# Kernel tuning notes

Hardware: AMD Instinct MI355X
Metric: run time of the kernel (lower is better)

## Reference

```python
import jax, jax.numpy as jnp
import numpy as np
from jax import lax

MAX_T = 1.0
MAX_Z = float(np.e)  # exp(MAX_T)
BITS = 8


def weight_quantization(w):
    # tanh -> scale by max-abs (no grad through alpha) -> clamp -> round with STE
    w = jnp.tanh(w)
    alpha = lax.stop_gradient(jnp.max(jnp.abs(w)))
    q = 2 ** (BITS - 1) - 1
    w = jnp.clip(w / alpha, -1.0, 1.0) * q
    w = w + lax.stop_gradient(jnp.round(w) - w)
    return w * alpha / q


def t_linear_c(inp, W, max_spike_time):
    # inp: [B, L, Fin], W: [Fout, Fin] -> out: [B, L, Fout]
    idx = jnp.argsort(inp, axis=-1)                              # [B,L,Fin]
    s_inp = jnp.take_along_axis(inp, idx, axis=-1)[..., None]    # [B,L,Fin,1]
    w_sorted = W.T[idx]                                          # [B,L,Fin,Fout]
    w_sorted = weight_quantization(w_sorted)
    mul = s_inp * w_sorted
    w_sum = jnp.cumsum(w_sorted, axis=-2)
    iw_sum = jnp.cumsum(mul, axis=-2)
    out_all = iw_sum / jnp.clip(w_sum - 1.0, 1e-10, 1e10)
    o = jnp.where(w_sum < 1.0, max_spike_time, out_all)
    o = jnp.where(o < s_inp, max_spike_time, o)
    nxt = jnp.concatenate([s_inp[:, :, 1:, :], jnp.ones_like(s_inp[:, :, :1, :])], axis=2)
    o = jnp.where(o > nxt, max_spike_time, o)
    return jnp.min(o, axis=-2)


def t_linear(inp, W, max_spike_time):
    # inp: [B, Fin], W: [Fout, Fin] -> out: [B, Fout]
    idx = jnp.argsort(inp, axis=-1)
    s_inp = jnp.take_along_axis(inp, idx, axis=-1)[..., None]    # [B,Fin,1]
    w_sorted = W.T[idx]                                          # [B,Fin,Fout]
    mul = s_inp * w_sorted
    w_sum = jnp.cumsum(w_sorted, axis=1)
    iw_sum = jnp.cumsum(mul, axis=1)
    out_all = iw_sum / jnp.clip(w_sum - 1.0, 1e-10, 1e10)
    o = jnp.where(w_sum < 1.0, max_spike_time, out_all)
    o = jnp.where(o < s_inp, max_spike_time, o)
    nxt = jnp.concatenate([s_inp[:, 1:, :], jnp.ones_like(s_inp[:, :1, :])], axis=1)
    o = jnp.where(o >= nxt, max_spike_time, o)  # note: >= in t_Linear (vs > in t_Linear_c)
    return jnp.min(o, axis=1)


def unfold(x, k, p, s):
    # torch F.unfold: zero-pad, extract kxk patches; feature order (C, kh, kw)
    B, C, H, W = x.shape
    xp = jnp.pad(x, ((0, 0), (0, 0), (p, p), (p, p)))
    oh = (H + 2 * p - k) // s + 1
    ow = (W + 2 * p - k) // s + 1
    ri = (jnp.arange(oh) * s)[:, None] + jnp.arange(k)           # [oh,k]
    ci = (jnp.arange(ow) * s)[:, None] + jnp.arange(k)           # [ow,k]
    pt = xp[:, :, ri[:, None, :, None], ci[None, :, None, :]]    # [B,C,oh,ow,k,k]
    pt = pt.transpose(0, 2, 3, 1, 4, 5).reshape(B, oh * ow, C * k * k)
    return pt, oh, ow


def t_conv(x, W, k, pad, stride, max_spike_time):
    B = x.shape[0]
    patches, oh, ow = unfold(x, k, pad, stride)                  # [B,L,C*k*k]
    patches = jnp.where(patches < 0.1, max_spike_time, patches)
    out = t_linear_c(patches, W, max_spike_time)                 # [B,L,Cout]
    return out.transpose(0, 2, 1).reshape(B, W.shape[0], oh, ow)


def max_pool2(x):
    return lax.reduce_window(x, -jnp.inf, lax.max, (1, 1, 2, 2), (1, 1, 2, 2), 'VALID')


def min_pool3(x):
    # -MaxPool3x3(stride 2)(-ConstantPad2d(1, 1e5)(x))
    xp = jnp.pad(x, ((0, 0), (0, 0), (1, 1), (1, 1)), constant_values=1e5)
    return -lax.reduce_window(-xp, -jnp.inf, lax.max, (1, 1, 3, 3), (1, 1, 2, 2), 'VALID')


def setup_inputs() -> dict:
    key = jax.random.key(0)
    ks = jax.random.split(key, 8)
    B = 8
    inp = jax.random.normal(ks[0], (B, 1, 64, 64), dtype=jnp.float32)
    conv1_w = jax.random.normal(ks[1], (32, 1, 5, 5), dtype=jnp.float32) * (1.0 / 5.0)
    bn_g = jnp.ones((32,), jnp.float32)
    bn_b = jnp.zeros((32,), jnp.float32)
    bn_m = jnp.zeros((32,), jnp.float32)
    bn_v = jnp.ones((32,), jnp.float32)
    def uw(k, fout, fin):
        return jax.random.uniform(k, (fout, fin), jnp.float32, 0.0, 10.0 / fin)
    w2 = uw(ks[2], 32, 3 * 3 * 32)
    w3 = uw(ks[3], 32, 3 * 3 * 32)
    w4 = uw(ks[4], 64, 3 * 3 * 32)
    w5 = uw(ks[5], 64, 3 * 3 * 64)
    w_fc = uw(ks[6], 10, 8 * 8 * 64)
    return {"inp": inp, "conv1_w": conv1_w, "bn_g": bn_g, "bn_b": bn_b,
            "bn_m": bn_m, "bn_v": bn_v, "w2": w2, "w3": w3, "w4": w4,
            "w5": w5, "w_fc": w_fc}


def reference(inp, conv1_w, bn_g, bn_b, bn_m, bn_v, w2, w3, w4, w5, w_fc):
    x = lax.conv_general_dilated(inp, conv1_w, (1, 1), ((2, 2), (2, 2)),
                                 dimension_numbers=('NCHW', 'OIHW', 'NCHW'))
    x = (x - bn_m[None, :, None, None]) * (bn_g / jnp.sqrt(bn_v + 1e-5))[None, :, None, None] \
        + bn_b[None, :, None, None]
    x = jax.nn.relu(x)
    x = max_pool2(x)                       # [B,32,32,32]
    x = jnp.minimum(x, MAX_T)
    z1 = jnp.exp(x)
    z2 = t_conv(z1, w2, 3, 1, 2, MAX_Z)    # [B,32,16,16]
    z3 = t_conv(z2, w3, 3, 1, 1, MAX_Z)    # [B,32,16,16]
    z3c = z3 * min_pool3(z1)
    z4 = t_conv(z3c, w4, 3, 1, 2, MAX_Z * 2)  # [B,64,8,8]
    z5 = t_conv(z4, w5, 3, 1, 1, MAX_Z * 2)   # [B,64,8,8]
    pm = min_pool3(z3c)                       # [B,32,8,8]
    pm = jnp.concatenate([pm, pm], axis=1)    # [B,64,8,8]
    z5c = (z5 * pm).reshape(z5.shape[0], -1)  # [B,4096]
    return t_linear(z5c, w_fc, MAX_Z * 4)     # [B,10]
```

## Files before the change

kernel.cpp:

```cpp
#include <hip/hip_runtime.h>
#include <hip/hip_bf16.h>
#include <math.h>

#define E32 2.7182817459106445f

__device__ __forceinline__ unsigned long long packkey(float vf, int idx) {
  unsigned u = __float_as_uint(vf);
  u = (u & 0x80000000u) ? ~u : (u | 0x80000000u);
  return (((unsigned long long)u) << 32) | (unsigned)idx;
}
__device__ __forceinline__ float unpackval(unsigned long long k) {
  unsigned m = (unsigned)(k >> 32);
  m = (m & 0x80000000u) ? (m ^ 0x80000000u) : ~m;
  return __uint_as_float(m);
}

__global__ __launch_bounds__(256) void tanh_max_kernel(
    const float* __restrict__ w2, const float* __restrict__ w3,
    const float* __restrict__ w4, const float* __restrict__ w5,
    float* __restrict__ tanhbuf, float* __restrict__ partials) {
  int blk = blockIdx.x;
  const float* w; int base_blk, tbase;
  if (blk < 36)       { w = w2; base_blk = 0;   tbase = 0; }
  else if (blk < 72)  { w = w3; base_blk = 36;  tbase = 9216; }
  else if (blk < 144) { w = w4; base_blk = 72;  tbase = 18432; }
  else                { w = w5; base_blk = 144; tbase = 36864; }
  int i = (blk - base_blk) * 256 + threadIdx.x;
  float t = tanhf(w[i]);
  tanhbuf[tbase + i] = t;
  __shared__ float red[256];
  red[threadIdx.x] = fabsf(t);
  __syncthreads();
  for (int s = 128; s > 0; s >>= 1) {
    if (threadIdx.x < s) red[threadIdx.x] = fmaxf(red[threadIdx.x], red[threadIdx.x + s]);
    __syncthreads();
  }
  if (threadIdx.x == 0) partials[blk] = red[0];
}

__global__ __launch_bounds__(256) void quant2_kernel(
    const float* __restrict__ tanhbuf, const float* __restrict__ partials,
    float* __restrict__ q2, float* __restrict__ q3,
    float* __restrict__ q4, float* __restrict__ q5) {
  int blk = blockIdx.x;
  float* dst; int base_blk, tbase, pb0, pb1, F, N;
  if (blk < 36)       { dst = q2; base_blk = 0;   tbase = 0;     pb0 = 0;   pb1 = 36;  F = 32; N = 288; }
  else if (blk < 72)  { dst = q3; base_blk = 36;  tbase = 9216;  pb0 = 36;  pb1 = 72;  F = 32; N = 288; }
  else if (blk < 144) { dst = q4; base_blk = 72;  tbase = 18432; pb0 = 72;  pb1 = 144; F = 64; N = 288; }
  else                { dst = q5; base_blk = 144; tbase = 36864; pb0 = 144; pb1 = 288; F = 64; N = 576; }
  __shared__ float red[256];
  float mx = 0.0f;
  for (int j = pb0 + threadIdx.x; j < pb1; j += 256) mx = fmaxf(mx, partials[j]);
  red[threadIdx.x] = mx;
  __syncthreads();
  for (int s = 128; s > 0; s >>= 1) {
    if (threadIdx.x < s) red[threadIdx.x] = fmaxf(red[threadIdx.x], red[threadIdx.x + s]);
    __syncthreads();
  }
  float a = red[0];
  int i = (blk - base_blk) * 256 + threadIdx.x;
  float t = tanhbuf[tbase + i];
  int f = i / N, n = i % N;
  float r = fminf(fmaxf(t / a, -1.0f), 1.0f) * 127.0f;
  dst[n * F + f] = rintf(r) * a / 127.0f;
}

__global__ __launch_bounds__(256) void transpose_wfc_kernel(
    const float* __restrict__ wfc, float* __restrict__ wfcT) {
  int o = blockIdx.x * 256 + threadIdx.x;
  if (o >= 40960) return;
  int n = o / 10, f = o % 10;
  wfcT[o] = wfc[f * 4096 + n];
}

__global__ __launch_bounds__(256) void conv1_kernel(
    const float* __restrict__ inp, const float* __restrict__ w,
    const float* __restrict__ g, const float* __restrict__ bb,
    const float* __restrict__ m, const float* __restrict__ vv,
    float* __restrict__ z1) {
  int idx = blockIdx.x * 256 + threadIdx.x;
  if (idx >= 8 * 32 * 32 * 32) return;
  int x = idx & 31, y = (idx >> 5) & 31, c = (idx >> 10) & 31, b = idx >> 15;
  float scale = g[c] / sqrtf(vv[c] + 1e-5f);
  float bias = bb[c];
  float mean = m[c];
  float mx = -3.402823466e38f;
  for (int dy = 0; dy < 2; ++dy) {
    for (int dx = 0; dx < 2; ++dx) {
      int oy = 2 * y + dy, ox = 2 * x + dx;
      float acc = 0.0f;
      for (int kh = 0; kh < 5; ++kh) {
        int r = oy + kh - 2;
        if (r < 0 || r >= 64) continue;
        for (int kw = 0; kw < 5; ++kw) {
          int cc2 = ox + kw - 2;
          if (cc2 < 0 || cc2 >= 64) continue;
          acc += w[c * 25 + kh * 5 + kw] * inp[(b * 64 + r) * 64 + cc2];
        }
      }
      float xs = (acc - mean) * scale + bias;
      xs = fmaxf(xs, 0.0f);
      mx = fmaxf(mx, xs);
    }
  }
  mx = fminf(mx, 1.0f);
  z1[idx] = (mx == 1.0f) ? E32 : expf(mx);
}

__global__ __launch_bounds__(256) void mp3_kernel(
    const float* __restrict__ in, float* __restrict__ out, int BC, int H) {
  int OH = H >> 1;
  int total = BC * OH * OH;
  int idx = blockIdx.x * 256 + threadIdx.x;
  if (idx >= total) return;
  int j = idx % OH, i = (idx / OH) % OH, bc = idx / (OH * OH);
  float mn = 100000.0f;
  for (int di = 0; di < 3; ++di) {
    int r = 2 * i - 1 + di;
    if (r < 0 || r >= H) continue;
    for (int dj = 0; dj < 3; ++dj) {
      int cc = 2 * j - 1 + dj;
      if (cc < 0 || cc >= H) continue;
      mn = fminf(mn, in[bc * H * H + r * H + cc]);
    }
  }
  out[idx] = mn;
}

__global__ __launch_bounds__(256) void mp3mul_kernel(
    const float* __restrict__ a, const float* __restrict__ b2,
    float* __restrict__ out, int BC, int H) {
  int OH = H >> 1;
  int total = BC * OH * OH;
  int idx = blockIdx.x * 256 + threadIdx.x;
  if (idx >= total) return;
  int j = idx % OH, i = (idx / OH) % OH, bc = idx / (OH * OH);
  float mn = 100000.0f;
  for (int di = 0; di < 3; ++di) {
    int r = 2 * i - 1 + di;
    if (r < 0 || r >= H) continue;
    for (int dj = 0; dj < 3; ++dj) {
      int cc = 2 * j - 1 + dj;
      if (cc < 0 || cc >= H) continue;
      int q = bc * H * H + r * H + cc;
      mn = fminf(mn, __fmul_rn(a[q], b2[q]));
    }
  }
  out[idx] = mn;
}

template <int CIN, int F, int S, int HIN, bool MUL, int T>
__global__ __launch_bounds__(T, 1) void tconv_kernel(
    const float* __restrict__ in, const float* __restrict__ in2,
    const float* __restrict__ wqt, float* __restrict__ out, float MST) {
  constexpr int N = CIN * 9;
  constexpr int OH = (HIN - 1) / S + 1;
  constexpr int P = OH * OH;
  constexpr int K = (N + T - 1) / T;
  constexpr int NCH = N / 32;

  __shared__ unsigned long long pk[N];
  __shared__ float sval[N + 1];
  __shared__ unsigned short sidx[N];
  __shared__ float wbuf[2][32 * F];
  __shared__ float wc[NCH][F];
  __shared__ float iwc[NCH][F];
  __shared__ float pmin[F * NCH];

  int blk = blockIdx.x;
  int b = blk / P, p = blk % P;
  int ph = p / OH, pw = p % OH;
  int tid = threadIdx.x;

  for (int n = tid; n < N; n += T) {
    int c = n / 9, kk = n % 9, kh = kk / 3, kw = kk % 3;
    int r = ph * S + kh - 1, cc = pw * S + kw - 1;
    float v = 0.0f;
    if (r >= 0 && r < HIN && cc >= 0 && cc < HIN) {
      int q = ((b * CIN + c) * HIN + r) * HIN + cc;
      v = MUL ? __fmul_rn(in[q], in2[q]) : in[q];
    }
    pk[n] = packkey((v < 0.1f) ? MST : v, n);
  }
  if (tid == 0) sval[N] = 1.0f;
  __syncthreads();

  unsigned long long mine[K];
  int rnk[K];
#pragma unroll
  for (int k = 0; k < K; ++k) {
    int i = tid + T * k;
    mine[k] = (i < N) ? pk[i] : ~0ull;
    rnk[k] = 0;
  }
  for (int j0 = 0; j0 < N; j0 += 8) {
    unsigned long long u[8];
#pragma unroll
    for (int r = 0; r < 8; ++r) u[r] = pk[j0 + r];
#pragma unroll
    for (int r = 0; r < 8; ++r) {
#pragma unroll
      for (int k = 0; k < K; ++k) rnk[k] += (u[r] < mine[k]) ? 1 : 0;
    }
  }
#pragma unroll
  for (int k = 0; k < K; ++k) {
    int i = tid + T * k;
    if (i < N) {
      sval[rnk[k]] = unpackval(mine[k]);
      sidx[rnk[k]] = (unsigned short)(mine[k] & 0xffffull);
    }
  }
  __syncthreads();

  for (int t = tid; t < 32 * F; t += T) {
    int q = t / F, f = t % F;
    wbuf[0][t] = wqt[(int)sidx[q] * F + f];
  }
  __syncthreads();

  float wsum = 0.0f, iwsum = 0.0f;
  for (int c = 0; c < NCH; ++c) {
    if (tid >= 64 && c + 1 < NCH) {
      int i0n = (c + 1) * 32;
      float* nb = wbuf[(c + 1) & 1];
      for (int t = tid - 64; t < 32 * F; t += (T - 64)) {
        int q = t / F, f = t % F;
        nb[t] = wqt[(int)sidx[i0n + q] * F + f];
      }
    }
    if (tid < F) {
      const float* wb = wbuf[c & 1];
      wc[c][tid] = wsum;
      iwc[c][tid] = iwsum;
      int i0 = c * 32;
#pragma unroll
      for (int q0 = 0; q0 < 32; q0 += 8) {
        float w8[8], s8[8];
#pragma unroll
        for (int r = 0; r < 8; ++r) {
          w8[r] = wb[(q0 + r) * F + tid];
          s8[r] = sval[i0 + q0 + r];
        }
#pragma unroll
        for (int r = 0; r < 8; ++r) {
          wsum = __fadd_rn(wsum, w8[r]);
          iwsum = __fadd_rn(iwsum, __fmul_rn(s8[r], w8[r]));
        }
      }
    }
    __syncthreads();
  }

  for (int task = tid; task < NCH * F; task += T) {
    int c = task / F, f = task % F;
    float ws = wc[c][f], iws = iwc[c][f], omin = 3.402823466e38f;
    int i0 = c * 32;
#pragma unroll
    for (int q0 = 0; q0 < 32; q0 += 8) {
      float wv8[8], sv8[8], nv8[8];
#pragma unroll
      for (int r = 0; r < 8; ++r) {
        int i = i0 + q0 + r;
        wv8[r] = wqt[(int)sidx[i] * F + f];
        sv8[r] = sval[i];
        nv8[r] = sval[i + 1];
      }
#pragma unroll
      for (int r = 0; r < 8; ++r) {
        ws = __fadd_rn(ws, wv8[r]);
        iws = __fadd_rn(iws, __fmul_rn(sv8[r], wv8[r]));
        float den = fminf(fmaxf(__fadd_rn(ws, -1.0f), 1e-10f), 1e10f);
        float oa = iws / den;
        float o = (ws < 1.0f) ? MST : oa;
        o = (o < sv8[r]) ? MST : o;
        o = (o > nv8[r]) ? MST : o;
        omin = fminf(omin, o);
      }
    }
    pmin[f * NCH + c] = omin;
  }
  __syncthreads();

  if (tid < F) {
    float m2 = pmin[tid * NCH];
#pragma unroll
    for (int c = 1; c < NCH; ++c) m2 = fminf(m2, pmin[tid * NCH + c]);
    out[(b * F + tid) * P + p] = m2;
  }
}

#define CE(x, y) { int i_ = (tid << 3) + (x); \
  bool up_ = (((i_ >> lk) & 1) == 0); \
  unsigned long long a_ = k[(x)], c_ = k[(y)]; \
  if ((a_ > c_) == up_) { k[(x)] = c_; k[(y)] = a_; } }

__global__ __launch_bounds__(512, 1) void fc_sort_kernel(
    const float* __restrict__ z5, const float* __restrict__ m3,
    float* __restrict__ svalG, unsigned short* __restrict__ sidxG) {
  __shared__ __align__(16) unsigned long long keys[4096];
  int b = blockIdx.x, tid = threadIdx.x, lane = tid & 63;

  unsigned long long k[8];
  {
    int c = tid >> 3, p0 = (tid << 3) & 63;
    const float4* z4p = (const float4*)(z5 + (b * 64 + c) * 64 + p0);
    const float4* m4p = (const float4*)(m3 + (b * 32 + (c & 31)) * 64 + p0);
    float4 za = z4p[0], zb = z4p[1], ma = m4p[0], mb = m4p[1];
    int n0 = tid << 3;
    k[0] = packkey(__fmul_rn(za.x, ma.x), n0 + 0);
    k[1] = packkey(__fmul_rn(za.y, ma.y), n0 + 1);
    k[2] = packkey(__fmul_rn(za.z, ma.z), n0 + 2);
    k[3] = packkey(__fmul_rn(za.w, ma.w), n0 + 3);
    k[4] = packkey(__fmul_rn(zb.x, mb.x), n0 + 4);
    k[5] = packkey(__fmul_rn(zb.y, mb.y), n0 + 5);
    k[6] = packkey(__fmul_rn(zb.z, mb.z), n0 + 6);
    k[7] = packkey(__fmul_rn(zb.w, mb.w), n0 + 7);
  }

  for (int lk = 1; lk <= 12; ++lk) {
    for (int lj = lk - 1; lj >= 0; --lj) {
      if (lj >= 9) {
        int pm = 1 << (lj - 3);
#pragma unroll
        for (int m = 0; m < 8; ++m) keys[m * 512 + tid] = k[m];
        __syncthreads();
        bool lower = ((tid & pm) == 0);
        bool up = (((tid >> (lk - 3)) & 1) == 0);
        bool wmin = (lower == up);
#pragma unroll
        for (int m = 0; m < 8; ++m) {
          unsigned long long o = keys[m * 512 + (tid ^ pm)];
          unsigned long long mine = k[m];
          k[m] = wmin ? (mine < o ? mine : o) : (mine > o ? mine : o);
        }
        __syncthreads();
      } else if (lj >= 3) {
        int lm = 1 << (lj - 3);
        bool lower = ((lane & lm) == 0);
        bool up = (((tid >> (lk - 3)) & 1) == 0);
        bool wmin = (lower == up);
#pragma unroll
        for (int m = 0; m < 8; ++m) {
          unsigned long long o = __shfl_xor(k[m], lm, 64);
          unsigned long long mine = k[m];
          k[m] = wmin ? (mine < o ? mine : o) : (mine > o ? mine : o);
        }
      } else if (lj == 2) {
        CE(0, 4) CE(1, 5) CE(2, 6) CE(3, 7)
      } else if (lj == 1) {
        CE(0, 2) CE(1, 3) CE(4, 6) CE(5, 7)
      } else {
        CE(0, 1) CE(2, 3) CE(4, 5) CE(6, 7)
      }
    }
  }

  {
    float4 v0, v1;
    v0.x = unpackval(k[0]); v0.y = unpackval(k[1]);
    v0.z = unpackval(k[2]); v0.w = unpackval(k[3]);
    v1.x = unpackval(k[4]); v1.y = unpackval(k[5]);
    v1.z = unpackval(k[6]); v1.w = unpackval(k[7]);
    float* svalRow = svalG + b * 4104;
    ((float4*)svalRow)[tid * 2] = v0;
    ((float4*)svalRow)[tid * 2 + 1] = v1;
    ushort si[8];
#pragma unroll
    for (int m = 0; m < 8; ++m) si[m] = (unsigned short)(k[m] & 0xffffull);
    ((ulong2*)(sidxG + b * 4096))[tid] = *(ulong2*)si;
    if (tid == 0) svalRow[4096] = 1.0f;
  }
}
#undef CE

__global__ __launch_bounds__(512, 1) void fc_scan_kernel(
    const float* __restrict__ svalG, const unsigned short* __restrict__ sidxG,
    const float* __restrict__ wfcT, float* __restrict__ out) {
  constexpr int NN = 4096;
  __shared__ __align__(16) float sval[NN + 1];
  __shared__ __align__(16) unsigned short sidx[NN];
  __shared__ __align__(16) float wstage[2][2608];
  __shared__ float wc[64][10];
  __shared__ float iwc[64][10];
  __shared__ float pmin[64][10];

  int b = blockIdx.x, tid = threadIdx.x;
  const float* svalRow = svalG + b * 4104;

  for (int t = tid; t < 1024; t += 512)
    ((float4*)sval)[t] = ((const float4*)svalRow)[t];
  ((ulong2*)sidx)[tid] = ((const ulong2*)(sidxG + b * 4096))[tid];
  if (tid == 0) sval[NN] = svalRow[4096];
  __syncthreads();

  {
    float tmp[5];
#pragma unroll
    for (int u = 0; u < 5; ++u) {
      int t = tid + u * 512;
      tmp[u] = wfcT[(int)sidx[t / 10] * 10 + (t % 10)];
    }
#pragma unroll
    for (int u = 0; u < 5; ++u) {
      int t = tid + u * 512;
      wstage[0][(t % 10) * 260 + t / 10] = tmp[u];
    }
  }
  __syncthreads();

  float wsum = 0.0f, iwsum = 0.0f;
  for (int c = 0; c < 16; ++c) {
    int c0 = c * 256;
    const float* cur = wstage[c & 1];
    float* nxt = wstage[(c & 1) ^ 1];
    if (tid >= 64 && c + 1 < 16) {
      int c0n = c0 + 256;
      float tmp[6];
#pragma unroll
      for (int u = 0; u < 6; ++u) {
        int t = (tid - 64) + u * 448;
        tmp[u] = (t < 2560) ? wfcT[(int)sidx[c0n + t / 10] * 10 + (t % 10)] : 0.0f;
      }
#pragma unroll
      for (int u = 0; u < 6; ++u) {
        int t = (tid - 64) + u * 448;
        if (t < 2560) nxt[(t % 10) * 260 + t / 10] = tmp[u];
      }
    }
    if (tid < 10) {
      const float* wrow = cur + tid * 260;
      float4 wA4[4], sA4[4], wB4[4], sB4[4];
      auto LD = [&](int i0, float4* w4, float4* s4) {
#pragma unroll
        for (int kq = 0; kq < 4; ++kq) {
          w4[kq] = *(const float4*)(wrow + i0 + 4 * kq);
          s4[kq] = *(const float4*)(sval + c0 + i0 + 4 * kq);
        }
      };
      auto ACC = [&](const float4* w4, const float4* s4) {
#pragma unroll
        for (int kq = 0; kq < 4; ++kq) {
          float w0 = w4[kq].x, w1 = w4[kq].y, w2 = w4[kq].z, w3 = w4[kq].w;
          float s0 = s4[kq].x, s1 = s4[kq].y, s2 = s4[kq].z, s3 = s4[kq].w;
          wsum = __fadd_rn(wsum, w0); iwsum = __fadd_rn(iwsum, __fmul_rn(s0, w0));
          wsum = __fadd_rn(wsum, w1); iwsum = __fadd_rn(iwsum, __fmul_rn(s1, w1));
          wsum = __fadd_rn(wsum, w2); iwsum = __fadd_rn(iwsum, __fmul_rn(s2, w2));
          wsum = __fadd_rn(wsum, w3); iwsum = __fadd_rn(iwsum, __fmul_rn(s3, w3));
        }
      };
      LD(0, wA4, sA4);
      for (int i0 = 0; i0 < 256; i0 += 32) {
        if ((i0 & 63) == 0) {
          int cc = (c0 + i0) >> 6;
          wc[cc][tid] = wsum;
          iwc[cc][tid] = iwsum;
        }
        LD(i0 + 16, wB4, sB4);
        ACC(wA4, sA4);
        if (i0 + 32 < 256) LD(i0 + 32, wA4, sA4);
        ACC(wB4, sB4);
      }
    }
    __syncthreads();
  }

  const float MST = 4.0f * E32;
  for (int task = tid; task < 640; task += 512) {
    int c = task / 10, f = task % 10;
    float wsr = wc[c][f], iwsr = iwc[c][f], omin = 3.402823466e38f;
    int i0 = c * 64;
    for (int q0 = 0; q0 < 64; q0 += 8) {
      float wv8[8], sv8[8], nv8[8];
#pragma unroll
      for (int r = 0; r < 8; ++r) {
        int i = i0 + q0 + r;
        wv8[r] = wfcT[(int)sidx[i] * 10 + f];
        sv8[r] = sval[i];
        nv8[r] = sval[i + 1];
      }
#pragma unroll
      for (int r = 0; r < 8; ++r) {
        wsr = __fadd_rn(wsr, wv8[r]);
        iwsr = __fadd_rn(iwsr, __fmul_rn(sv8[r], wv8[r]));
        float den = fminf(fmaxf(__fadd_rn(wsr, -1.0f), 1e-10f), 1e10f);
        float oa = iwsr / den;
        float o = (wsr < 1.0f) ? MST : oa;
        o = (o < sv8[r]) ? MST : o;
        o = (o >= nv8[r]) ? MST : o;
        omin = fminf(omin, o);
      }
    }
    pmin[c][f] = omin;
  }
  __syncthreads();

  if (tid < 10) {
    float m = pmin[0][tid];
#pragma unroll
    for (int c = 1; c < 64; ++c) m = fminf(m, pmin[c][tid]);
    out[b * 10 + tid] = m;
  }
}

extern "C" void kernel_launch(void* const* d_in, const int* in_sizes, int n_in,
                              void* d_out, int out_size, void* d_ws, size_t ws_size,
                              hipStream_t stream) {
  const float* inp   = (const float*)d_in[0];
  const float* w1    = (const float*)d_in[1];
  const float* bn_g  = (const float*)d_in[2];
  const float* bn_b  = (const float*)d_in[3];
  const float* bn_m  = (const float*)d_in[4];
  const float* bn_v  = (const float*)d_in[5];
  const float* w2    = (const float*)d_in[6];
  const float* w3    = (const float*)d_in[7];
  const float* w4    = (const float*)d_in[8];
  const float* w5    = (const float*)d_in[9];
  const float* wfc   = (const float*)d_in[10];
  float* out = (float*)d_out;

  float* ws = (float*)d_ws;
  float* wq2 = ws + 16;
  float* wq3 = wq2 + 9216;
  float* wq4 = wq3 + 9216;
  float* wq5 = wq4 + 18432;
  float* z1  = wq5 + 36864;
  float* m1  = z1 + 262144;
  float* z2  = m1 + 65536;
  float* z3  = z2 + 65536;
  float* m3  = z3 + 65536;
  float* z4  = m3 + 16384;
  float* z5  = z4 + 32768;
  float* tanhbuf  = z5 + 32768;
  float* partials = tanhbuf + 73728;
  float* wfcT = partials + 512;
  float* svalG = wfcT + 40960;
  unsigned short* sidxG = (unsigned short*)(svalG + 32832);

  tanh_max_kernel<<<288, 256, 0, stream>>>(w2, w3, w4, w5, tanhbuf, partials);
  quant2_kernel<<<288, 256, 0, stream>>>(tanhbuf, partials, wq2, wq3, wq4, wq5);
  transpose_wfc_kernel<<<160, 256, 0, stream>>>(wfc, wfcT);

  conv1_kernel<<<1024, 256, 0, stream>>>(inp, w1, bn_g, bn_b, bn_m, bn_v, z1);
  mp3_kernel<<<256, 256, 0, stream>>>(z1, m1, 8 * 32, 32);

  tconv_kernel<32, 32, 2, 32, false, 320><<<8 * 256, 320, 0, stream>>>(z1, nullptr, wq2, z2, E32);
  tconv_kernel<32, 32, 1, 16, false, 320><<<8 * 256, 320, 0, stream>>>(z2, nullptr, wq3, z3, E32);
  mp3mul_kernel<<<64, 256, 0, stream>>>(z3, m1, m3, 8 * 32, 16);
  tconv_kernel<32, 64, 2, 16, true, 512><<<8 * 64, 512, 0, stream>>>(z3, m1, wq4, z4, 2.0f * E32);
  tconv_kernel<64, 64, 1, 8, false, 512><<<8 * 64, 512, 0, stream>>>(z4, nullptr, wq5, z5, 2.0f * E32);

  fc_sort_kernel<<<8, 512, 0, stream>>>(z5, m3, svalG, sidxG);
  fc_scan_kernel<<<8, 512, 0, stream>>>(svalG, sidxG, wfcT, out);
}
```

Baseline: 265.2 us.

## Replace rank-count sort with bitonic sort in tconv and fuse small kernels

The per-pixel sort in the temporal conv kernels changes from an O(N^2) rank-counting sort to a bitonic sort on padded keys. It uses wavefront shuffles for short strides and shared memory with barriers for long strides. All tconv launches now use 512 threads. The weight-transpose kernel is merged into the quantization launch, and the FC sort and scan kernels are fused so the sorted data stays in shared memory, cutting launches and a global round trip. The bitonic network adds many block-wide barriers and pads N up to 512 or 1024 elements.

```diff
diff --git a/kernel.cpp b/kernel.cpp
--- a/kernel.cpp
+++ b/kernel.cpp
@@ -38,11 +38,20 @@
   if (threadIdx.x == 0) partials[blk] = red[0];
 }
 
-__global__ __launch_bounds__(256) void quant2_kernel(
+__global__ __launch_bounds__(256) void quantT_kernel(
     const float* __restrict__ tanhbuf, const float* __restrict__ partials,
     float* __restrict__ q2, float* __restrict__ q3,
-    float* __restrict__ q4, float* __restrict__ q5) {
+    float* __restrict__ q4, float* __restrict__ q5,
+    const float* __restrict__ wfc, float* __restrict__ wfcT) {
   int blk = blockIdx.x;
+  if (blk >= 288) {
+    int o = (blk - 288) * 256 + threadIdx.x;
+    if (o < 40960) {
+      int n = o / 10, f = o % 10;
+      wfcT[o] = wfc[f * 4096 + n];
+    }
+    return;
+  }
   float* dst; int base_blk, tbase, pb0, pb1, F, N;
   if (blk < 36)       { dst = q2; base_blk = 0;   tbase = 0;     pb0 = 0;   pb1 = 36;  F = 32; N = 288; }
   else if (blk < 72)  { dst = q3; base_blk = 36;  tbase = 9216;  pb0 = 36;  pb1 = 72;  F = 32; N = 288; }
@@ -63,14 +72,6 @@
   int f = i / N, n = i % N;
   float r = fminf(fmaxf(t / a, -1.0f), 1.0f) * 127.0f;
   dst[n * F + f] = rintf(r) * a / 127.0f;
-}
-
-__global__ __launch_bounds__(256) void transpose_wfc_kernel(
-    const float* __restrict__ wfc, float* __restrict__ wfcT) {
-  int o = blockIdx.x * 256 + threadIdx.x;
-  if (o >= 40960) return;
-  int n = o / 10, f = o % 10;
-  wfcT[o] = wfc[f * 4096 + n];
 }
 
 __global__ __launch_bounds__(256) void conv1_kernel(
@@ -149,17 +150,19 @@
   out[idx] = mn;
 }
 
-template <int CIN, int F, int S, int HIN, bool MUL, int T>
-__global__ __launch_bounds__(T, 1) void tconv_kernel(
+template <int CIN, int F, int S, int HIN, bool MUL>
+__global__ __launch_bounds__(512, 1) void tconv_kernel(
     const float* __restrict__ in, const float* __restrict__ in2,
     const float* __restrict__ wqt, float* __restrict__ out, float MST) {
   constexpr int N = CIN * 9;
+  constexpr int NP = (N <= 512) ? 512 : 1024;
+  constexpr int KP = NP / 512;
   constexpr int OH = (HIN - 1) / S + 1;
   constexpr int P = OH * OH;
-  constexpr int K = (N + T - 1) / T;
+  constexpr int T = 512;
   constexpr int NCH = N / 32;
 
-  __shared__ unsigned long long pk[N];
+  __shared__ __align__(16) unsigned long long pk[NP];
   __shared__ float sval[N + 1];
   __shared__ unsigned short sidx[N];
   __shared__ float wbuf[2][32 * F];
@@ -172,43 +175,81 @@
   int ph = p / OH, pw = p % OH;
   int tid = threadIdx.x;
 
-  for (int n = tid; n < N; n += T) {
-    int c = n / 9, kk = n % 9, kh = kk / 3, kw = kk % 3;
-    int r = ph * S + kh - 1, cc = pw * S + kw - 1;
-    float v = 0.0f;
-    if (r >= 0 && r < HIN && cc >= 0 && cc < HIN) {
-      int q = ((b * CIN + c) * HIN + r) * HIN + cc;
-      v = MUL ? __fmul_rn(in[q], in2[q]) : in[q];
-    }
-    pk[n] = packkey((v < 0.1f) ? MST : v, n);
+  for (int n = tid; n < NP; n += T) {
+    if (n < N) {
+      int c = n / 9, kk = n % 9, kh = kk / 3, kw = kk % 3;
+      int r = ph * S + kh - 1, cc = pw * S + kw - 1;
+      float v = 0.0f;
+      if (r >= 0 && r < HIN && cc >= 0 && cc < HIN) {
+        int q = ((b * CIN + c) * HIN + r) * HIN + cc;
+        v = MUL ? __fmul_rn(in[q], in2[q]) : in[q];
+      }
+      pk[n] = packkey((v < 0.1f) ? MST : v, n);
+    } else {
+      pk[n] = ~0ull;
+    }
   }
   if (tid == 0) sval[N] = 1.0f;
   __syncthreads();
 
-  unsigned long long mine[K];
-  int rnk[K];
-#pragma unroll
-  for (int k = 0; k < K; ++k) {
-    int i = tid + T * k;
-    mine[k] = (i < N) ? pk[i] : ~0ull;
-    rnk[k] = 0;
-  }
-  for (int j0 = 0; j0 < N; j0 += 8) {
-    unsigned long long u[8];
-#pragma unroll
-    for (int r = 0; r < 8; ++r) u[r] = pk[j0 + r];
-#pragma unroll
-    for (int r = 0; r < 8; ++r) {
-#pragma unroll
-      for (int k = 0; k < K; ++k) rnk[k] += (u[r] < mine[k]) ? 1 : 0;
-    }
-  }
-#pragma unroll
-  for (int k = 0; k < K; ++k) {
-    int i = tid + T * k;
-    if (i < N) {
-      sval[rnk[k]] = unpackval(mine[k]);
-      sidx[rnk[k]] = (unsigned short)(mine[k] & 0xffffull);
+  if constexpr (KP == 1) {
+    unsigned long long k0 = pk[tid];
+    __syncthreads();
+    for (int lk = 1; lk <= 9; ++lk) {
+      for (int lj = lk - 1; lj >= 0; --lj) {
+        int j = 1 << lj;
+        bool up = ((tid >> lk) & 1) == 0;
+        bool wmin = (((tid & j) == 0) == up);
+        unsigned long long o;
+        if (lj >= 6) {
+          pk[tid] = k0;
+          __syncthreads();
+          o = pk[tid ^ j];
+          __syncthreads();
+        } else {
+          o = __shfl_xor(k0, j, 64);
+        }
+        k0 = wmin ? (k0 < o ? k0 : o) : (k0 > o ? k0 : o);
+      }
+    }
+    if (tid < N) {
+      sval[tid] = unpackval(k0);
+      sidx[tid] = (unsigned short)(k0 & 0xffffull);
+    }
+  } else {
+    unsigned long long k0 = pk[2 * tid], k1 = pk[2 * tid + 1];
+    __syncthreads();
+    for (int lk = 1; lk <= 10; ++lk) {
+      for (int lj = lk - 1; lj >= 0; --lj) {
+        bool up = ((tid >> (lk - 1)) & 1) == 0;
+        if (lj == 0) {
+          if ((k0 > k1) == up) { unsigned long long t2 = k0; k0 = k1; k1 = t2; }
+        } else {
+          int tj = 1 << (lj - 1);
+          bool wmin = (((tid & tj) == 0) == up);
+          unsigned long long o0, o1;
+          if (lj >= 7) {
+            pk[tid] = k0; pk[512 + tid] = k1;
+            __syncthreads();
+            o0 = pk[tid ^ tj]; o1 = pk[512 + (tid ^ tj)];
+            __syncthreads();
+          } else {
+            o0 = __shfl_xor(k0, tj, 64);
+            o1 = __shfl_xor(k1, tj, 64);
+          }
+          k0 = wmin ? (k0 < o0 ? k0 : o0) : (k0 > o0 ? k0 : o0);
+          k1 = wmin ? (k1 < o1 ? k1 : o1) : (k1 > o1 ? k1 : o1);
+        }
+      }
+    }
+    int i0 = tid * 2;
+    if (i0 < N) {
+      sval[i0] = unpackval(k0);
+      sidx[i0] = (unsigned short)(k0 & 0xffffull);
+    }
+    if (i0 + 1 < N) {
+      sval[i0 + 1] = unpackval(k1);
+      sidx[i0 + 1] = (unsigned short)(k1 & 0xffffull);
     }
   }
   __syncthreads();
@@ -295,10 +336,19 @@
   unsigned long long a_ = k[(x)], c_ = k[(y)]; \
   if ((a_ > c_) == up_) { k[(x)] = c_; k[(y)] = a_; } }
 
-__global__ __launch_bounds__(512, 1) void fc_sort_kernel(
+__global__ __launch_bounds__(512, 1) void fc_kernel(
     const float* __restrict__ z5, const float* __restrict__ m3,
-    float* __restrict__ svalG, unsigned short* __restrict__ sidxG) {
-  __shared__ __align__(16) unsigned long long keys[4096];
+    const float* __restrict__ wfcT, float* __restrict__ out) {
+  constexpr int NN = 4096;
+  __shared__ __align__(16) unsigned long long keys[NN];
+  __shared__ __align__(16) float sval[NN + 1];
+  __shared__ __align__(16) unsigned short sidx[NN];
+  __shared__ float wc[64][10];
+  __shared__ float iwc[64][10];
+  __shared__ float pmin[64][10];
+  float* wsA = (float*)keys;
+  float* wsB = (float*)keys + 2608;
+
   int b = blockIdx.x, tid = threadIdx.x, lane = tid & 63;
 
   unsigned long long k[8];
@@ -362,36 +412,14 @@
     v0.z = unpackval(k[2]); v0.w = unpackval(k[3]);
     v1.x = unpackval(k[4]); v1.y = unpackval(k[5]);
     v1.z = unpackval(k[6]); v1.w = unpackval(k[7]);
-    float* svalRow = svalG + b * 4104;
-    ((float4*)svalRow)[tid * 2] = v0;
-    ((float4*)svalRow)[tid * 2 + 1] = v1;
+    ((float4*)sval)[tid * 2] = v0;
+    ((float4*)sval)[tid * 2 + 1] = v1;
     ushort si[8];
 #pragma unroll
     for (int m = 0; m < 8; ++m) si[m] = (unsigned short)(k[m] & 0xffffull);
-    ((ulong2*)(sidxG + b * 4096))[tid] = *(ulong2*)si;
-    if (tid == 0) svalRow[4096] = 1.0f;
-  }
-}
-#undef CE
-
-__global__ __launch_bounds__(512, 1) void fc_scan_kernel(
-    const float* __restrict__ svalG, const unsigned short* __restrict__ sidxG,
-    const float* __restrict__ wfcT, float* __restrict__ out) {
-  constexpr int NN = 4096;
-  __shared__ __align__(16) float sval[NN + 1];
-  __shared__ __align__(16) unsigned short sidx[NN];
-  __shared__ __align__(16) float wstage[2][2608];
-  __shared__ float wc[64][10];
-  __shared__ float iwc[64][10];
-  __shared__ float pmin[64][10];
-
-  int b = blockIdx.x, tid = threadIdx.x;
-  const float* svalRow = svalG + b * 4104;
-
-  for (int t = tid; t < 1024; t += 512)
-    ((float4*)sval)[t] = ((const float4*)svalRow)[t];
-  ((ulong2*)sidx)[tid] = ((const ulong2*)(sidxG + b * 4096))[tid];
-  if (tid == 0) sval[NN] = svalRow[4096];
+    ((ulong2*)sidx)[tid] = *(ulong2*)si;
+  }
+  if (tid == 0) sval[NN] = 1.0f;
   __syncthreads();
 
   {
@@ -404,7 +432,7 @@
 #pragma unroll
     for (int u = 0; u < 5; ++u) {
       int t = tid + u * 512;
-      wstage[0][(t % 10) * 260 + t / 10] = tmp[u];
+      wsA[(t % 10) * 260 + t / 10] = tmp[u];
     }
   }
   __syncthreads();
@@ -412,8 +440,8 @@
   float wsum = 0.0f, iwsum = 0.0f;
   for (int c = 0; c < 16; ++c) {
     int c0 = c * 256;
-    const float* cur = wstage[c & 1];
-    float* nxt = wstage[(c & 1) ^ 1];
+    float* cur = (c & 1) ? wsB : wsA;
+    float* nxt = (c & 1) ? wsA : wsB;
     if (tid >= 64 && c + 1 < 16) {
       int c0n = c0 + 256;
       float tmp[6];
@@ -502,6 +530,7 @@
     out[b * 10 + tid] = m;
   }
 }
+#undef CE
 
 extern "C" void kernel_launch(void* const* d_in, const int* in_sizes, int n_in,
                               void* d_out, int out_size, void* d_ws, size_t ws_size,
@@ -534,22 +563,18 @@
   float* tanhbuf  = z5 + 32768;
   float* partials = tanhbuf + 73728;
   float* wfcT = partials + 512;
-  float* svalG = wfcT + 40960;
-  unsigned short* sidxG = (unsigned short*)(svalG + 32832);
 
   tanh_max_kernel<<<288, 256, 0, stream>>>(w2, w3, w4, w5, tanhbuf, partials);
-  quant2_kernel<<<288, 256, 0, stream>>>(tanhbuf, partials, wq2, wq3, wq4, wq5);
-  transpose_wfc_kernel<<<160, 256, 0, stream>>>(wfc, wfcT);
+  quantT_kernel<<<448, 256, 0, stream>>>(tanhbuf, partials, wq2, wq3, wq4, wq5, wfc, wfcT);
 
   conv1_kernel<<<1024, 256, 0, stream>>>(inp, w1, bn_g, bn_b, bn_m, bn_v, z1);
   mp3_kernel<<<256, 256, 0, stream>>>(z1, m1, 8 * 32, 32);
 
-  tconv_kernel<32, 32, 2, 32, false, 320><<<8 * 256, 320, 0, stream>>>(z1, nullptr, wq2, z2, E32);
-  tconv_kernel<32, 32, 1, 16, false, 320><<<8 * 256, 320, 0, stream>>>(z2, nullptr, wq3, z3, E32);
+  tconv_kernel<32, 32, 2, 32, false><<<8 * 256, 512, 0, stream>>>(z1, nullptr, wq2, z2, E32);
+  tconv_kernel<32, 32, 1, 16, false><<<8 * 256, 512, 0, stream>>>(z2, nullptr, wq3, z3, E32);
   mp3mul_kernel<<<64, 256, 0, stream>>>(z3, m1, m3, 8 * 32, 16);
-  tconv_kernel<32, 64, 2, 16, true, 512><<<8 * 64, 512, 0, stream>>>(z3, m1, wq4, z4, 2.0f * E32);
-  tconv_kernel<64, 64, 1, 8, false, 512><<<8 * 64, 512, 0, stream>>>(z4, nullptr, wq5, z5, 2.0f * E32);
-
-  fc_sort_kernel<<<8, 512, 0, stream>>>(z5, m3, svalG, sidxG);
-  fc_scan_kernel<<<8, 512, 0, stream>>>(svalG, sidxG, wfcT, out);
-}
+  tconv_kernel<32, 64, 2, 16, true><<<8 * 64, 512, 0, stream>>>(z3, m1, wq4, z4, 2.0f * E32);
+  tconv_kernel<64, 64, 1, 8, false><<<8 * 64, 512, 0, stream>>>(z4, nullptr, wq5, z5, 2.0f * E32);
+
+  fc_kernel<<<8, 512, 0, stream>>>(z5, m3, wfcT, out);
+}
```

Result: faster. 255.3 us (-3.7%).
